# Kernel tuning notes

Measured on AMD Instinct MI355X. Metric: run time of the kernel, lower is better.

The kernel has to match this reference:

```python
import jax, jax.numpy as jnp
import numpy as np

D_IN = 1024
D_OUT = 1024
NUM_HEADS = 16
DIM_HEAD = D_OUT // NUM_HEADS


def setup_inputs() -> dict:
    key = jax.random.key(0)
    ks = jax.random.split(key, 6)
    s = 0.02
    x = jax.random.normal(ks[0], (2, 2048, D_IN), dtype=jnp.float32)
    Wk = jax.random.normal(ks[1], (D_IN, D_OUT), dtype=jnp.float32) * s
    Wq = jax.random.normal(ks[2], (D_IN, D_OUT), dtype=jnp.float32) * s
    Wv = jax.random.normal(ks[3], (D_IN, D_OUT), dtype=jnp.float32) * s
    Wo = jax.random.normal(ks[4], (D_OUT, D_OUT), dtype=jnp.float32) * s
    bo = jax.random.normal(ks[5], (D_OUT,), dtype=jnp.float32) * s
    return {"x": x, "Wk": Wk, "Wq": Wq, "Wv": Wv, "Wo": Wo, "bo": bo}


def reference(x, Wk, Wq, Wv, Wo, bo):
    B, S, _ = x.shape
    # projections -> [B, H, S, Dh]
    def split_heads(t):
        return t.reshape(B, S, NUM_HEADS, DIM_HEAD).transpose(0, 2, 1, 3)
    q = split_heads(x @ Wq)
    k = split_heads(x @ Wk)
    v = split_heads(x @ Wv)
    # NOTE: source uses non-in-place masked_fill whose result is discarded,
    # so NO causal mask is actually applied (faithful reproduction).
    scores = jnp.einsum("bhqd,bhkd->bhqk", q, k) / jnp.sqrt(jnp.float32(DIM_HEAD))
    wgts = jax.nn.softmax(scores, axis=-1)  # dropout = identity (eval mode)
    ctx = jnp.einsum("bhqk,bhkd->bhqd", wgts, v)
    ctx = ctx.transpose(0, 2, 1, 3).reshape(B, S, D_OUT)
    return ctx @ Wo + bo
```

## Files before the change

### kernel.cpp

```cpp
#include <hip/hip_runtime.h>
#include <stdint.h>

typedef short bf16x8 __attribute__((ext_vector_type(8)));
typedef float f32x4  __attribute__((ext_vector_type(4)));
typedef unsigned int u32x4 __attribute__((ext_vector_type(4)));
typedef unsigned int u32x2 __attribute__((ext_vector_type(2)));

__device__ __forceinline__ unsigned short f2bf(float f) {
  unsigned int u = __builtin_bit_cast(unsigned int, f) + 0x8000u;
  return (unsigned short)(u >> 16);
}
__device__ __forceinline__ unsigned int pack2bf(float a, float b) {
  unsigned int ua = __builtin_bit_cast(unsigned int, a) + 0x8000u;
  unsigned int ub = __builtin_bit_cast(unsigned int, b) + 0x8000u;
  return __builtin_amdgcn_perm(ub, ua, 0x07060302);
}
__device__ __forceinline__ unsigned int cvtpk2bf(float a, float b) {
  unsigned int r;
  asm("v_cvt_pk_bf16_f32 %0, %1, %2" : "=v"(r) : "v"(a), "v"(b));
  return r;
}

__device__ __forceinline__ void gl2lds16(const void* g, void* l) {
  __builtin_amdgcn_global_load_lds(
      (const __attribute__((address_space(1))) void*)g,
      (__attribute__((address_space(3))) void*)l, 16, 0, 0);
}

template <int N> __device__ __forceinline__ void wait_vmcnt() {
  asm volatile("s_waitcnt vmcnt(%0)" ::"n"(N) : "memory");
}

__global__ __launch_bounds__(256) void cast_fused_k(
    const float* __restrict__ x, unsigned short* __restrict__ xb,
    const float* __restrict__ Wq, const float* __restrict__ Wk,
    const float* __restrict__ Wv, const float* __restrict__ Wo,
    unsigned short* __restrict__ Tq, unsigned short* __restrict__ Tk,
    unsigned short* __restrict__ Tv, unsigned short* __restrict__ To) {
  __shared__ float tile[32][33];
  const int tid = threadIdx.x;
  const int bid = blockIdx.x;
  if (bid < 4096) {
    int i = bid * 256 + tid;
    float4 v = ((const float4*)x)[i];
    u32x2 o;
    o.x = pack2bf(v.x, v.y);
    o.y = pack2bf(v.z, v.w);
    ((u32x2*)xb)[i] = o;
  } else {
    const int bb = bid - 4096;
    const int z = bb >> 10, rem = bb & 1023;
    const float* W = (z == 0) ? Wq : (z == 1) ? Wk : (z == 2) ? Wv : Wo;
    unsigned short* T = (z == 0) ? Tq : (z == 1) ? Tk : (z == 2) ? Tv : To;
    const int tx = tid & 31, ty = tid >> 5;
    const int n0 = (rem & 31) * 32, k0 = (rem >> 5) * 32;
#pragma unroll
    for (int j = 0; j < 32; j += 8)
      tile[ty + j][tx] = W[(size_t)(k0 + ty + j) * 1024 + n0 + tx];
    __syncthreads();
#pragma unroll
    for (int j = 0; j < 32; j += 8)
      T[(size_t)(n0 + ty + j) * 1024 + k0 + tx] = f2bf(tile[tx][ty + j]);
  }
}

template <int MODE, int TN, int WN, int NTHR>
__global__ __launch_bounds__(NTHR, 2) void gemm_bt_k(const unsigned short* __restrict__ A,
                                                     const unsigned short* __restrict__ B,
                                                     void* __restrict__ C,
                                                     const float* __restrict__ bias,
                                                     int K) {
  constexpr int BN = WN * TN * 16;
  constexpr int ALD = 512 / NTHR;
  constexpr int BLD = BN * 4 / NTHR;
  constexpr int PT = ALD + BLD;
  __shared__ alignas(16) short lA[4][512 * 8];
  __shared__ alignas(16) short lB[4][BN * 4 * 8];
  const int tid = threadIdx.x;
  const int wid = tid >> 6, lane = tid & 63;
  const int l15 = lane & 15, quad = lane >> 4;
  const int waveM = wid / WN, waveN = wid % WN;
  const int bm = blockIdx.y * 128, bn = blockIdx.x * BN;

  f32x4 acc[4][TN];
#pragma unroll
  for (int i = 0; i < 4; ++i)
#pragma unroll
    for (int j = 0; j < TN; ++j) acc[i][j] = (f32x4){0.f, 0.f, 0.f, 0.f};

  auto stage = [&](int kk, short* la, short* lb) {
#pragma unroll
    for (int j = 0; j < ALD; ++j) {
      int c = tid + NTHR * j;
      int row = ((c >> 6) << 4) | (c & 15);
      int ch = (c >> 4) & 3;
      gl2lds16(A + (size_t)(bm + row) * K + kk + ch * 8, &la[(c & ~63) * 8]);
    }
#pragma unroll
    for (int j = 0; j < BLD; ++j) {
      int c = tid + NTHR * j;
      int row = ((c >> 6) << 4) | (c & 15);
      int ch = (c >> 4) & 3;
      gl2lds16(B + (size_t)(bn + row) * K + kk + ch * 8, &lb[(c & ~63) * 8]);
    }
  };

  auto compute = [&](const short* la, const short* lb) {
    bf16x8 af[4], bfr[TN];
#pragma unroll
    for (int i = 0; i < 4; ++i)
      af[i] = *(const bf16x8*)&la[(((waveM * 4 + i) * 64) + lane) * 8];
#pragma unroll
    for (int j = 0; j < TN; ++j)
      bfr[j] = *(const bf16x8*)&lb[(((waveN * TN + j) * 64) + lane) * 8];
    __builtin_amdgcn_s_setprio(1);
#pragma unroll
    for (int i = 0; i < 4; ++i)
#pragma unroll
      for (int j = 0; j < TN; ++j)
        acc[i][j] = __builtin_amdgcn_mfma_f32_16x16x32_bf16(af[i], bfr[j], acc[i][j], 0, 0, 0);
    __builtin_amdgcn_s_setprio(0);
  };

  const int NT = K >> 5;
  short *pa0 = lA[0], *pa1 = lA[1], *pa2 = lA[2], *pa3 = lA[3];
  short *pb0 = lB[0], *pb1 = lB[1], *pb2 = lB[2], *pb3 = lB[3];
  stage(0, pa0, pb0);
  stage(32, pa1, pb1);
#pragma unroll 1
  for (int t = 0; t < NT - 2; ++t) {
    stage((t + 2) * 32, pa2, pb2);
    wait_vmcnt<2 * PT>();
    __builtin_amdgcn_sched_barrier(0);
    __builtin_amdgcn_s_barrier();
    __builtin_amdgcn_sched_barrier(0);
    compute(pa0, pb0);
    short* ta = pa0; pa0 = pa1; pa1 = pa2; pa2 = pa3; pa3 = ta;
    short* tb = pb0; pb0 = pb1; pb1 = pb2; pb2 = pb3; pb3 = tb;
  }
  wait_vmcnt<PT>();
  __builtin_amdgcn_sched_barrier(0);
  __builtin_amdgcn_s_barrier();
  __builtin_amdgcn_sched_barrier(0);
  compute(pa0, pb0);
  { short* ta = pa0; pa0 = pa1; pa1 = pa2; pa2 = pa3; pa3 = ta;
    short* tb = pb0; pb0 = pb1; pb1 = pb2; pb2 = pb3; pb3 = tb; }
  wait_vmcnt<0>();
  __builtin_amdgcn_sched_barrier(0);
  __builtin_amdgcn_s_barrier();
  __builtin_amdgcn_sched_barrier(0);
  compute(pa0, pb0);

#pragma unroll
  for (int i = 0; i < 4; ++i)
#pragma unroll
    for (int j = 0; j < TN; ++j) {
      int row = bm + waveM * 64 + i * 16 + quad * 4;
      int col = bn + (waveN * TN + j) * 16 + l15;
      if (MODE == 0) {
        unsigned short* Cq = (unsigned short*)C;
        int w = col >> 10, n1 = col & 1023;
        int h = n1 >> 6, d = n1 & 63;
        int b = row >> 11, s = row & 2047;
        int bhh = (b << 4) + h;
        if (w == 2) {
          int g = (i << 2) + quad;
          int ks2 = g >> 3, rem = g & 7;
          int pos = ((ks2 << 2) + (rem & 3)) * 8 + (rem >> 2) * 4;
          u32x2 pk;
          pk.x = pack2bf(acc[i][j][0], acc[i][j][1]);
          pk.y = pack2bf(acc[i][j][2], acc[i][j][3]);
          *(u32x2*)&Cq[(size_t)2 * 4194304 + ((size_t)bhh * 64 + d) * 2048 +
                       (s & ~63) + pos] = pk;
        } else {
          float sc = (w == 0) ? 0.18033688011112042f : 1.0f;
#pragma unroll
          for (int r = 0; r < 4; ++r)
            Cq[(size_t)w * 4194304 + ((size_t)bhh * 2048 + s + r) * 64 + d] =
                f2bf(acc[i][j][r] * sc);
        }
      } else {
#pragma unroll
        for (int r = 0; r < 4; ++r)
          ((float*)C)[(size_t)(row + r) * 1024 + col] = acc[i][j][r] + bias[col];
      }
    }
}

__global__ __launch_bounds__(512, 2) void gemm_pair_k(const unsigned short* __restrict__ A,
                                                      const unsigned short* __restrict__ B,
                                                      float* __restrict__ C,
                                                      const float* __restrict__ bias,
                                                      int K) {
  constexpr int TN = 2;
  __shared__ alignas(16) short lA[8][512 * 8];
  __shared__ alignas(16) short lB[8][512 * 8];
  const int tid = threadIdx.x;
  const int wid = tid >> 6, lane = tid & 63;
  const int l15 = lane & 15, quad = lane >> 4;
  const int waveM = wid >> 2, waveN = wid & 3;
  const int bm = blockIdx.y * 128, bn = blockIdx.x * 128;

  f32x4 acc[4][TN];
#pragma unroll
  for (int i = 0; i < 4; ++i)
#pragma unroll
    for (int j = 0; j < TN; ++j) acc[i][j] = (f32x4){0.f, 0.f, 0.f, 0.f};

  auto stage = [&](int kk, short* la, short* lb) {
    int c = tid;
    int row = ((c >> 6) << 4) | (c & 15);
    int ch = (c >> 4) & 3;
    gl2lds16(A + (size_t)(bm + row) * K + kk + ch * 8, &la[(c & ~63) * 8]);
    gl2lds16(B + (size_t)(bn + row) * K + kk + ch * 8, &lb[(c & ~63) * 8]);
  };

  auto compute = [&](const short* la, const short* lb) {
    bf16x8 af[4], bfr[TN];
#pragma unroll
    for (int i = 0; i < 4; ++i)
      af[i] = *(const bf16x8*)&la[(((waveM * 4 + i) * 64) + lane) * 8];
#pragma unroll
    for (int j = 0; j < TN; ++j)
      bfr[j] = *(const bf16x8*)&lb[(((waveN * TN + j) * 64) + lane) * 8];
    __builtin_amdgcn_s_setprio(1);
#pragma unroll
    for (int i = 0; i < 4; ++i)
#pragma unroll
      for (int j = 0; j < TN; ++j)
        acc[i][j] = __builtin_amdgcn_mfma_f32_16x16x32_bf16(af[i], bfr[j], acc[i][j], 0, 0, 0);
    __builtin_amdgcn_s_setprio(0);
  };

  const int NP = K >> 6;
  short *a0 = lA[0], *a1 = lA[1], *a2 = lA[2], *a3 = lA[3],
        *a4 = lA[4], *a5 = lA[5], *a6 = lA[6], *a7 = lA[7];
  short *b0 = lB[0], *b1 = lB[1], *b2 = lB[2], *b3 = lB[3],
        *b4 = lB[4], *b5 = lB[5], *b6 = lB[6], *b7 = lB[7];
  stage(0, a0, b0);  stage(32, a1, b1);
  stage(64, a2, b2); stage(96, a3, b3);
#pragma unroll 1
  for (int p = 0; p < NP - 2; ++p) {
    stage((2 * p + 4) * 32, a4, b4);
    stage((2 * p + 5) * 32, a5, b5);
    wait_vmcnt<8>();
    __builtin_amdgcn_sched_barrier(0);
    __builtin_amdgcn_s_barrier();
    __builtin_amdgcn_sched_barrier(0);
    compute(a0, b0);
    compute(a1, b1);
    short* t;
    t = a0; a0 = a2; a2 = a4; a4 = a6; a6 = t;
    t = a1; a1 = a3; a3 = a5; a5 = a7; a7 = t;
    t = b0; b0 = b2; b2 = b4; b4 = b6; b6 = t;
    t = b1; b1 = b3; b3 = b5; b5 = b7; b7 = t;
  }
  wait_vmcnt<4>();
  __builtin_amdgcn_sched_barrier(0);
  __builtin_amdgcn_s_barrier();
  __builtin_amdgcn_sched_barrier(0);
  compute(a0, b0);
  compute(a1, b1);
  { short* t;
    t = a0; a0 = a2; a2 = a4; a4 = a6; a6 = t;
    t = a1; a1 = a3; a3 = a5; a5 = a7; a7 = t;
    t = b0; b0 = b2; b2 = b4; b4 = b6; b6 = t;
    t = b1; b1 = b3; b3 = b5; b5 = b7; b7 = t; }
  wait_vmcnt<0>();
  __builtin_amdgcn_sched_barrier(0);
  __builtin_amdgcn_s_barrier();
  __builtin_amdgcn_sched_barrier(0);
  compute(a0, b0);
  compute(a1, b1);

#pragma unroll
  for (int i = 0; i < 4; ++i)
#pragma unroll
    for (int j = 0; j < TN; ++j) {
      int row = bm + waveM * 64 + i * 16 + quad * 4;
      int col = bn + (waveN * TN + j) * 16 + l15;
#pragma unroll
      for (int r = 0; r < 4; ++r)
        C[(size_t)(row + r) * 1024 + col] = acc[i][j][r] + bias[col];
    }
}

__global__ __launch_bounds__(256, 2) void flash_k(const unsigned short* __restrict__ Qh,
                                                  const unsigned short* __restrict__ Kh,
                                                  const unsigned short* __restrict__ Vt,
                                                  unsigned short* __restrict__ ctxb) {
  constexpr int SL = 2048;
  __shared__ alignas(16) short kt[4][512 * 8];
  __shared__ alignas(16) short vt[4][512 * 8];

  const int tid = threadIdx.x;
  const int wid = tid >> 6, lane = tid & 63;
  const int l15 = lane & 15, quad = lane >> 4;
  const int bid = blockIdx.x;
  const int jj = bid >> 3;
  const int bh = ((bid & 7) << 2) | (jj >> 4);
  const int q0 = (jj & 15) * 128 + wid * 32;

  const unsigned short* Qb = Qh + (size_t)bh * SL * 64;
  const unsigned short* Kb = Kh + (size_t)bh * SL * 64;
  const unsigned short* Vb = Vt + (size_t)bh * 64 * SL;

  bf16x8 qf[2][2];
#pragma unroll
  for (int s = 0; s < 2; ++s)
#pragma unroll
    for (int ks = 0; ks < 2; ++ks)
      qf[s][ks] = *(const bf16x8*)(Qb + (size_t)(q0 + s * 16 + l15) * 64 + ks * 32 + quad * 8);

  f32x4 o[2][4];
  f32x4 rs4[2] = {(f32x4){0.f, 0.f, 0.f, 0.f}, (f32x4){0.f, 0.f, 0.f, 0.f}};
  const f32x4 z4 = (f32x4){0.f, 0.f, 0.f, 0.f};
#pragma unroll
  for (int s = 0; s < 2; ++s)
#pragma unroll
    for (int t = 0; t < 4; ++t) o[s][t] = z4;

  auto stage = [&](int kb, short* ktb, short* vtb) {
#pragma unroll
    for (int j2 = 0; j2 < 2; ++j2) {
      int cc = tid + 256 * j2;
      int row = cc >> 3;
      int ko = (cc & 7) ^ (row & 7);
      gl2lds16(Kb + (size_t)(kb + row) * 64 + ko * 8, &ktb[(cc & ~63) * 8]);
      gl2lds16(Vb + (size_t)row * SL + kb + ko * 8, &vtb[(cc & ~63) * 8]);
    }
  };

  auto computeQK = [&](const short* ktb, f32x4 (&sv)[2][4]) {
    __builtin_amdgcn_s_setprio(1);
#pragma unroll
    for (int t = 0; t < 4; ++t) {
      int key = t * 16 + l15;
      bf16x8 kf0 = *(bf16x8*)&ktb[(key * 8 + (quad ^ (key & 7))) * 8];
      bf16x8 kf1 = *(bf16x8*)&ktb[(key * 8 + ((4 + quad) ^ (key & 7))) * 8];
#pragma unroll
      for (int s = 0; s < 2; ++s) {
        sv[s][t] = __builtin_amdgcn_mfma_f32_16x16x32_bf16(kf0, qf[s][0], z4, 0, 0, 0);
        sv[s][t] = __builtin_amdgcn_mfma_f32_16x16x32_bf16(kf1, qf[s][1], sv[s][t], 0, 0, 0);
      }
    }
    __builtin_amdgcn_s_setprio(0);
  };

  auto computeSMPV = [&](const short* vtb, f32x4 (&sv)[2][4]) {
    u32x4 pf[2][2];
#pragma unroll
    for (int s = 0; s < 2; ++s)
#pragma unroll
      for (int t = 0; t < 4; ++t) {
        f32x4 p;
#pragma unroll
        for (int r = 0; r < 4; ++r) p[r] = __builtin_amdgcn_exp2f(sv[s][t][r]);
        rs4[s] += p;
        pf[s][t >> 1][(t & 1) * 2 + 0] = cvtpk2bf(p[0], p[1]);
        pf[s][t >> 1][(t & 1) * 2 + 1] = cvtpk2bf(p[2], p[3]);
      }
    __builtin_amdgcn_s_setprio(1);
#pragma unroll
    for (int t = 0; t < 4; ++t) {
      int d = t * 16 + l15;
#pragma unroll
      for (int ks = 0; ks < 2; ++ks) {
        bf16x8 vf = *(bf16x8*)&vtb[(d * 8 + ((ks * 4 + quad) ^ (d & 7))) * 8];
#pragma unroll
        for (int s = 0; s < 2; ++s)
          o[s][t] = __builtin_amdgcn_mfma_f32_16x16x32_bf16(
              vf, __builtin_bit_cast(bf16x8, pf[s][ks]), o[s][t], 0, 0, 0);
      }
    }
    __builtin_amdgcn_s_setprio(0);
  };

  short *kA0 = kt[0], *kA1 = kt[1], *kB0 = kt[2], *kB1 = kt[3];
  short *vA0 = vt[0], *vA1 = vt[1], *vB0 = vt[2], *vB1 = vt[3];
  stage(0, kA0, vA0);
  stage(64, kA1, vA1);
#pragma unroll 1
  for (int i2 = 0; i2 < 16; ++i2) {
    wait_vmcnt<0>();
    __builtin_amdgcn_sched_barrier(0);
    __builtin_amdgcn_s_barrier();
    __builtin_amdgcn_sched_barrier(0);
    if (i2 < 15) {
      stage((2 * i2 + 2) * 64, kB0, vB0);
      stage((2 * i2 + 3) * 64, kB1, vB1);
    }
    f32x4 sv0[2][4], sv1[2][4];
    computeQK(kA0, sv0);
    computeQK(kA1, sv1);
    computeSMPV(vA0, sv0);
    computeSMPV(vA1, sv1);
    short* t;
    t = kA0; kA0 = kB0; kB0 = t;  t = kA1; kA1 = kB1; kB1 = t;
    t = vA0; vA0 = vB0; vB0 = t;  t = vA1; vA1 = vB1; vB1 = t;
  }

  const int bb = bh >> 4, h = bh & 15;
#pragma unroll
  for (int s = 0; s < 2; ++s) {
    float v = (rs4[s][0] + rs4[s][1]) + (rs4[s][2] + rs4[s][3]);
    v += __shfl_xor(v, 16);
    v += __shfl_xor(v, 32);
    float inv = 1.0f / v;
    int tok = q0 + s * 16 + l15;
    size_t base = ((size_t)(bb * 2048 + tok)) * 1024 + h * 64;
#pragma unroll
    for (int t = 0; t < 4; ++t) {
      u32x2 pk;
      pk.x = pack2bf(o[s][t][0] * inv, o[s][t][1] * inv);
      pk.y = pack2bf(o[s][t][2] * inv, o[s][t][3] * inv);
      *(u32x2*)&ctxb[base + t * 16 + quad * 4] = pk;
    }
  }
}

extern "C" void kernel_launch(void* const* d_in, const int* in_sizes, int n_in,
                              void* d_out, int out_size, void* d_ws, size_t ws_size,
                              hipStream_t stream) {
  const float* x  = (const float*)d_in[0];
  const float* Wk = (const float*)d_in[1];
  const float* Wq = (const float*)d_in[2];
  const float* Wv = (const float*)d_in[3];
  const float* Wo = (const float*)d_in[4];
  const float* bo = (const float*)d_in[5];
  float* out = (float*)d_out;

  char* ws = (char*)d_ws;
  const size_t MB = 1u << 20;
  unsigned short* xb   = (unsigned short*)(ws);
  unsigned short* WqT  = (unsigned short*)(ws + 8  * MB);
  unsigned short* WkT  = (unsigned short*)(ws + 10 * MB);
  unsigned short* WvT  = (unsigned short*)(ws + 12 * MB);
  unsigned short* WoT  = (unsigned short*)(ws + 14 * MB);
  unsigned short* Qh   = (unsigned short*)(ws + 16 * MB);
  unsigned short* ctxb = xb;

  cast_fused_k<<<8192, 256, 0, stream>>>(x, xb, Wq, Wk, Wv, Wo, WqT, WkT, WvT, WoT);
  gemm_bt_k<0, 6, 4, 512><<<dim3(8, 32), 512, 0, stream>>>(xb, WqT, Qh, nullptr, 1024);
  flash_k<<<512, 256, 0, stream>>>(Qh, Qh + 4194304, Qh + 2 * 4194304, ctxb);
  gemm_pair_k<<<dim3(8, 32), 512, 0, stream>>>(ctxb, WoT, out, bo, 1024);
}
```

Measured before the change: 184.1 us.

## Replace QKV projection GEMM with 256x256-tile kernel and double-buffered K=64 staging

Swaps the templated 128x384-tile QKV GEMM for a dedicated kernel that computes 256x256 output tiles per block, with each wave holding an 8x4 grid of MFMA accumulators. The K loop now stages two 32-wide slices per step into a double buffer, so there are fewer barriers per K and more reuse of the data held in LDS. The aim is higher arithmetic intensity and fewer LDS/global loads per flop. In exchange the grid shrinks to 192 blocks, which may underfill the GPU, and register pressure rises with 32 accumulator tiles per wave, risking spills or lower occupancy.

Result: slower. 199.7 us (+8.5%).

```diff
diff --git a/kernel.cpp b/kernel.cpp
--- a/kernel.cpp
+++ b/kernel.cpp
@@ -64,125 +64,105 @@
   }
 }
 
-template <int MODE, int TN, int WN, int NTHR>
-__global__ __launch_bounds__(NTHR, 2) void gemm_bt_k(const unsigned short* __restrict__ A,
-                                                     const unsigned short* __restrict__ B,
-                                                     void* __restrict__ C,
-                                                     const float* __restrict__ bias,
-                                                     int K) {
-  constexpr int BN = WN * TN * 16;
-  constexpr int ALD = 512 / NTHR;
-  constexpr int BLD = BN * 4 / NTHR;
-  constexpr int PT = ALD + BLD;
-  __shared__ alignas(16) short lA[4][512 * 8];
-  __shared__ alignas(16) short lB[4][BN * 4 * 8];
+__global__ __launch_bounds__(512, 2) void gemm_qkv8_k(const unsigned short* __restrict__ A,
+                                                      const unsigned short* __restrict__ B,
+                                                      unsigned short* __restrict__ Cq) {
+  constexpr int K = 1024;
+  __shared__ alignas(16) short lA[2][2][1024 * 8];
+  __shared__ alignas(16) short lB[2][2][1024 * 8];
   const int tid = threadIdx.x;
   const int wid = tid >> 6, lane = tid & 63;
   const int l15 = lane & 15, quad = lane >> 4;
-  const int waveM = wid / WN, waveN = wid % WN;
-  const int bm = blockIdx.y * 128, bn = blockIdx.x * BN;
-
-  f32x4 acc[4][TN];
-#pragma unroll
-  for (int i = 0; i < 4; ++i)
-#pragma unroll
-    for (int j = 0; j < TN; ++j) acc[i][j] = (f32x4){0.f, 0.f, 0.f, 0.f};
-
-  auto stage = [&](int kk, short* la, short* lb) {
-#pragma unroll
-    for (int j = 0; j < ALD; ++j) {
-      int c = tid + NTHR * j;
+  const int waveM = wid >> 2, waveN = wid & 3;
+  const int bm = blockIdx.y * 256, bn = blockIdx.x * 256;
+
+  f32x4 acc[8][4];
+#pragma unroll
+  for (int m = 0; m < 8; ++m)
+#pragma unroll
+    for (int n = 0; n < 4; ++n) acc[m][n] = (f32x4){0.f, 0.f, 0.f, 0.f};
+
+  auto stageHalf = [&](const unsigned short* X, int xoff, int kk, short* dst) {
+#pragma unroll
+    for (int j = 0; j < 2; ++j) {
+      int c = tid + 512 * j;
       int row = ((c >> 6) << 4) | (c & 15);
       int ch = (c >> 4) & 3;
-      gl2lds16(A + (size_t)(bm + row) * K + kk + ch * 8, &la[(c & ~63) * 8]);
-    }
-#pragma unroll
-    for (int j = 0; j < BLD; ++j) {
-      int c = tid + NTHR * j;
-      int row = ((c >> 6) << 4) | (c & 15);
-      int ch = (c >> 4) & 3;
-      gl2lds16(B + (size_t)(bn + row) * K + kk + ch * 8, &lb[(c & ~63) * 8]);
-    }
-  };
-
-  auto compute = [&](const short* la, const short* lb) {
-    bf16x8 af[4], bfr[TN];
-#pragma unroll
-    for (int i = 0; i < 4; ++i)
-      af[i] = *(const bf16x8*)&la[(((waveM * 4 + i) * 64) + lane) * 8];
-#pragma unroll
-    for (int j = 0; j < TN; ++j)
-      bfr[j] = *(const bf16x8*)&lb[(((waveN * TN + j) * 64) + lane) * 8];
-    __builtin_amdgcn_s_setprio(1);
-#pragma unroll
-    for (int i = 0; i < 4; ++i)
-#pragma unroll
-      for (int j = 0; j < TN; ++j)
-        acc[i][j] = __builtin_amdgcn_mfma_f32_16x16x32_bf16(af[i], bfr[j], acc[i][j], 0, 0, 0);
-    __builtin_amdgcn_s_setprio(0);
-  };
-
-  const int NT = K >> 5;
-  short *pa0 = lA[0], *pa1 = lA[1], *pa2 = lA[2], *pa3 = lA[3];
-  short *pb0 = lB[0], *pb1 = lB[1], *pb2 = lB[2], *pb3 = lB[3];
-  stage(0, pa0, pb0);
-  stage(32, pa1, pb1);
+      gl2lds16(X + (size_t)(xoff + row) * K + kk + ch * 8, &dst[(c & ~63) * 8]);
+    }
+  };
+
+  stageHalf(A, bm, 0, lA[0][0]);
+  stageHalf(B, bn, 0, lB[0][0]);
+  stageHalf(A, bm, 32, lA[0][1]);
+  stageHalf(B, bn, 32, lB[0][1]);
+
 #pragma unroll 1
-  for (int t = 0; t < NT - 2; ++t) {
-    stage((t + 2) * 32, pa2, pb2);
-    wait_vmcnt<2 * PT>();
-    __builtin_amdgcn_sched_barrier(0);
-    __builtin_amdgcn_s_barrier();
-    __builtin_amdgcn_sched_barrier(0);
-    compute(pa0, pb0);
-    short* ta = pa0; pa0 = pa1; pa1 = pa2; pa2 = pa3; pa3 = ta;
-    short* tb = pb0; pb0 = pb1; pb1 = pb2; pb2 = pb3; pb3 = tb;
+  for (int t = 0; t < 16; ++t) {
+    const int buf = t & 1, nb = buf ^ 1;
+    const int nk = ((t + 1) & 15) * 64;
+#pragma unroll
+    for (int ks = 0; ks < 2; ++ks) {
+      wait_vmcnt<4>();
+      __builtin_amdgcn_sched_barrier(0);
+      __builtin_amdgcn_s_barrier();
+      __builtin_amdgcn_sched_barrier(0);
+      stageHalf(A, bm, nk + ks * 32, &lA[nb][ks][0]);
+      stageHalf(B, bn, nk + ks * 32, &lB[nb][ks][0]);
+      const short* la = &lA[buf][ks][0];
+      const short* lb = &lB[buf][ks][0];
+      bf16x8 bfr[4], af[4], af2[4];
+#pragma unroll
+      for (int n = 0; n < 4; ++n)
+        bfr[n] = *(const bf16x8*)&lb[(((waveN * 4 + n) * 64) + lane) * 8];
+#pragma unroll
+      for (int m = 0; m < 4; ++m)
+        af[m] = *(const bf16x8*)&la[(((waveM * 8 + m) * 64) + lane) * 8];
+      __builtin_amdgcn_s_setprio(1);
+#pragma unroll
+      for (int m = 0; m < 4; ++m)
+#pragma unroll
+        for (int n = 0; n < 4; ++n)
+          acc[m][n] = __builtin_amdgcn_mfma_f32_16x16x32_bf16(af[m], bfr[n], acc[m][n], 0, 0, 0);
+      __builtin_amdgcn_s_setprio(0);
+#pragma unroll
+      for (int m = 0; m < 4; ++m)
+        af2[m] = *(const bf16x8*)&la[(((waveM * 8 + 4 + m) * 64) + lane) * 8];
+      __builtin_amdgcn_s_setprio(1);
+#pragma unroll
+      for (int m = 0; m < 4; ++m)
+#pragma unroll
+        for (int n = 0; n < 4; ++n)
+          acc[4 + m][n] = __builtin_amdgcn_mfma_f32_16x16x32_bf16(af2[m], bfr[n], acc[4 + m][n], 0, 0, 0);
+      __builtin_amdgcn_s_setprio(0);
+    }
   }
-  wait_vmcnt<PT>();
-  __builtin_amdgcn_sched_barrier(0);
-  __builtin_amdgcn_s_barrier();
-  __builtin_amdgcn_sched_barrier(0);
-  compute(pa0, pb0);
-  { short* ta = pa0; pa0 = pa1; pa1 = pa2; pa2 = pa3; pa3 = ta;
-    short* tb = pb0; pb0 = pb1; pb1 = pb2; pb2 = pb3; pb3 = tb; }
-  wait_vmcnt<0>();
-  __builtin_amdgcn_sched_barrier(0);
-  __builtin_amdgcn_s_barrier();
-  __builtin_amdgcn_sched_barrier(0);
-  compute(pa0, pb0);
-
-#pragma unroll
-  for (int i = 0; i < 4; ++i)
-#pragma unroll
-    for (int j = 0; j < TN; ++j) {
-      int row = bm + waveM * 64 + i * 16 + quad * 4;
-      int col = bn + (waveN * TN + j) * 16 + l15;
-      if (MODE == 0) {
-        unsigned short* Cq = (unsigned short*)C;
-        int w = col >> 10, n1 = col & 1023;
-        int h = n1 >> 6, d = n1 & 63;
-        int b = row >> 11, s = row & 2047;
-        int bhh = (b << 4) + h;
-        if (w == 2) {
-          int g = (i << 2) + quad;
-          int ks2 = g >> 3, rem = g & 7;
-          int pos = ((ks2 << 2) + (rem & 3)) * 8 + (rem >> 2) * 4;
-          u32x2 pk;
-          pk.x = pack2bf(acc[i][j][0], acc[i][j][1]);
-          pk.y = pack2bf(acc[i][j][2], acc[i][j][3]);
-          *(u32x2*)&Cq[(size_t)2 * 4194304 + ((size_t)bhh * 64 + d) * 2048 +
-                       (s & ~63) + pos] = pk;
-        } else {
-          float sc = (w == 0) ? 0.18033688011112042f : 1.0f;
-#pragma unroll
-          for (int r = 0; r < 4; ++r)
-            Cq[(size_t)w * 4194304 + ((size_t)bhh * 2048 + s + r) * 64 + d] =
-                f2bf(acc[i][j][r] * sc);
-        }
+
+#pragma unroll
+  for (int m = 0; m < 8; ++m)
+#pragma unroll
+    for (int n = 0; n < 4; ++n) {
+      int row = bm + waveM * 128 + m * 16 + quad * 4;
+      int col = bn + waveN * 64 + n * 16 + l15;
+      int w = col >> 10, n1 = col & 1023;
+      int h = n1 >> 6, d = n1 & 63;
+      int b = row >> 11, s = row & 2047;
+      int bhh = (b << 4) + h;
+      if (w == 2) {
+        int g = ((m & 3) << 2) | quad;
+        int ks2 = g >> 3, rem = g & 7;
+        int pos = ((ks2 << 2) + (rem & 3)) * 8 + (rem >> 2) * 4;
+        u32x2 pk;
+        pk.x = pack2bf(acc[m][n][0], acc[m][n][1]);
+        pk.y = pack2bf(acc[m][n][2], acc[m][n][3]);
+        *(u32x2*)&Cq[(size_t)2 * 4194304 + ((size_t)bhh * 64 + d) * 2048 +
+                     (s & ~63) + pos] = pk;
       } else {
+        float sc = (w == 0) ? 0.18033688011112042f : 1.0f;
 #pragma unroll
         for (int r = 0; r < 4; ++r)
-          ((float*)C)[(size_t)(row + r) * 1024 + col] = acc[i][j][r] + bias[col];
+          Cq[(size_t)w * 4194304 + ((size_t)bhh * 2048 + s + r) * 64 + d] =
+              f2bf(acc[m][n][r] * sc);
       }
     }
 }
@@ -441,7 +421,7 @@
   unsigned short* ctxb = xb;
 
   cast_fused_k<<<8192, 256, 0, stream>>>(x, xb, Wq, Wk, Wv, Wo, WqT, WkT, WvT, WoT);
-  gemm_bt_k<0, 6, 4, 512><<<dim3(8, 32), 512, 0, stream>>>(xb, WqT, Qh, nullptr, 1024);
+  gemm_qkv8_k<<<dim3(12, 16), 512, 0, stream>>>(xb, WqT, Qh);
   flash_k<<<512, 256, 0, stream>>>(Qh, Qh + 4194304, Qh + 2 * 4194304, ctxb);
   gemm_pair_k<<<dim3(8, 32), 512, 0, stream>>>(ctxb, WoT, out, bo, 1024);
 }
```
